# Kernel optimization log

Measured on AMD Instinct MI355X. Metric: run time of the kernel, lower is better.

Reference implementation:

```python
import jax, jax.numpy as jnp
import numpy as np

EPS = 1e-8

def squash(s, axis=-1):
    sq = jnp.sum(s * s, axis=axis, keepdims=True)
    return sq / (1.0 + sq) * s / (jnp.sqrt(sq) + EPS)

def setup_inputs() -> dict:
    key = jax.random.key(0)
    k1, k2 = jax.random.split(key)
    B, in_caps, in_dim = 256, 1152, 8
    num_caps, dim_caps = 10, 16
    x = jax.random.normal(k1, (B, in_caps, in_dim), dtype=jnp.float32)
    W = 0.01 * jax.random.normal(k2, (num_caps, in_caps, dim_caps, in_dim), dtype=jnp.float32)
    return {"x": x, "W": W}

def reference(x, W, num_routing=3):
    # u_hat: [B, num_caps, in_caps, dim_caps]
    u_hat = jnp.einsum('ncdi,bci->bncd', W, x)
    u_hat_det = jax.lax.stop_gradient(u_hat)
    B, N, C, D = u_hat.shape
    b = jnp.zeros((B, N, C, 1), dtype=u_hat.dtype)
    for _ in range(num_routing - 1):
        c = jax.nn.softmax(b, axis=1)                 # over num_caps
        s = jnp.sum(c * u_hat_det, axis=2)            # [B, N, D]
        v = squash(s)
        uv = jnp.einsum('bncd,bnd->bnc', u_hat_det, v)[..., None]
        b = b + uv
    c = jax.nn.softmax(b, axis=1)
    s = jnp.sum(c * u_hat, axis=2)
    v = squash(s)                                     # [B, N, D]
    return v
```

## Files before the change

kernel.cpp:

```cpp
#include <hip/hip_runtime.h>
#include <math.h>
#include <stdint.h>

#define B_N 256
#define C_N 1152
#define I_N 8
#define N_N 10
#define D_N 16

constexpr int C_PER    = 18;
constexpr int C_CHUNKS = C_N / C_PER;
constexpr int STAGE_C  = 3;
constexpr int N_STAGES = 6;
constexpr int BLOCK    = 256;

typedef short v8s __attribute__((ext_vector_type(8)));
typedef float v4f __attribute__((ext_vector_type(4)));

constexpr int POOL_BYTES = 32432;

constexpr size_t VSTG_FL = 16 * 16 * 164;
constexpr size_t PS_FL   = (size_t)C_CHUNKS * B_N * 160;
constexpr size_t WB_SH   = (size_t)C_N * 1280;
constexpr int    BAR_W   = 16 * 64;

#define GLD16(g, l)                                                         \
    __builtin_amdgcn_global_load_lds(                                       \
        (const uint32_t __attribute__((address_space(1)))*)(g),             \
        (uint32_t __attribute__((address_space(3)))*)(l), 16, 0, 0)

__device__ __forceinline__ void st16_sc1(float* p, v4f v) {
    asm volatile("global_store_dwordx4 %0, %1, off sc1"
                 :: "v"(p), "v"(v) : "memory");
}
__device__ __forceinline__ v4f ld16_sc1(const float* p) {
    v4f v;
    asm volatile("global_load_dwordx4 %0, %1, off sc1\n\t"
                 "s_waitcnt vmcnt(0)"
                 : "=&v"(v) : "v"(p) : "memory");
    return v;
}

__device__ __forceinline__ uint32_t cvtpk(float a, float b) {
    uint32_t r;
    asm("v_cvt_pk_bf16_f32 %0, %1, %2" : "=v"(r) : "v"(a), "v"(b));
    return r;
}
__device__ __forceinline__ float bf2f(short s) {
    return __uint_as_float(((uint32_t)(uint16_t)s) << 16);
}

__global__ __launch_bounds__(BLOCK)
void conv_all(const float* __restrict__ W, short* __restrict__ Wb,
              uint32_t* __restrict__ bar)
{
    if (blockIdx.x == 0) {
        for (int i = threadIdx.x; i < BAR_W; i += BLOCK) bar[i] = 0u;
    }
    const int c0 = blockIdx.x * 8;
    const int cc = threadIdx.x >> 5;
    const int k4 = threadIdx.x & 31;
    const float4* W4 = (const float4*)W;
    uint2* dst = (uint2*)Wb;
    for (int n = 0; n < N_N; ++n) {
        float4 v = W4[(size_t)n * 36864 + (size_t)(c0 + cc) * 32 + k4];
        dst[(((size_t)(c0 + cc) * 1280 + n * 128) >> 2) + k4] =
            make_uint2(cvtpk(v.x, v.y), cvtpk(v.z, v.w));
    }
}

__device__ __forceinline__ void gbar(uint32_t* bar, int group, uint32_t expect)
{
    asm volatile("s_waitcnt vmcnt(0) lgkmcnt(0)" ::: "memory");
    __syncthreads();
    if (threadIdx.x == 0) {
        uint32_t* cnt = &bar[group * 64];
        uint32_t* ph  = &bar[group * 64 + 32];
        uint32_t a = __hip_atomic_fetch_add(cnt, 1u, __ATOMIC_RELAXED,
                                            __HIP_MEMORY_SCOPE_AGENT);
        if (a == 63u) {
            __hip_atomic_store(cnt, 0u, __ATOMIC_RELAXED,
                               __HIP_MEMORY_SCOPE_AGENT);
            asm volatile("s_waitcnt vmcnt(0)" ::: "memory");
            __hip_atomic_fetch_add(ph, 1u, __ATOMIC_RELAXED,
                                   __HIP_MEMORY_SCOPE_AGENT);
        }
        while (__hip_atomic_load(ph, __ATOMIC_RELAXED,
                                 __HIP_MEMORY_SCOPE_AGENT) < expect)
            __builtin_amdgcn_s_sleep(2);
    }
    __syncthreads();
}

template <bool FIRST>
__device__ __forceinline__ void route_core(
    short* wbuf, const short* xs, float* vst, float* cfl, float* comb,
    const short* __restrict__ Wb, const float* __restrict__ vstG,
    float* __restrict__ p_s, int chunk, int btile)
{
    const int tid  = threadIdx.x;
    const int wv   = tid >> 6;
    const int lane = tid & 63;
    const int b    = lane & 15;
    const int quad = lane >> 4;
    const int gb0  = btile * 16;
    const int c0   = chunk * C_PER;

    if (!FIRST) {
        const float* src = vstG + (size_t)btile * 2624;
        const int f0 = tid;
        const int f1 = tid + 256;
        int f2 = tid + 512; f2 = (f2 < 656) ? f2 : 655;
        v4f t0, t1, t2;
        asm volatile(
            "global_load_dwordx4 %0, %3, off sc1\n\t"
            "global_load_dwordx4 %1, %4, off sc1\n\t"
            "global_load_dwordx4 %2, %5, off sc1\n\t"
            "s_waitcnt vmcnt(0)"
            : "=&v"(t0), "=&v"(t1), "=&v"(t2)
            : "v"(src + f0 * 4), "v"(src + f1 * 4), "v"(src + f2 * 4)
            : "memory");
        *(v4f*)((char*)vst + f0 * 16) = t0;
        *(v4f*)((char*)vst + f1 * 16) = t1;
        *(v4f*)((char*)vst + f2 * 16) = t2;
    }
    #pragma unroll
    for (int s0 = 0; s0 < 2; ++s0) {
        const char* src = (const char*)(Wb + (size_t)(c0 + s0 * STAGE_C) * 1280);
        char* dst = (char*)(wbuf + s0 * (STAGE_C * 1280));
        #pragma unroll
        for (int it = 0; it < 2; ++it) {
            int f = tid + BLOCK * it;
            if (f < 480) GLD16(src + f * 16, dst + f * 16);
        }
        asm volatile("" ::: "memory");
    }
    asm volatile("s_waitcnt vmcnt(2) lgkmcnt(0)" ::: "memory");
    __builtin_amdgcn_s_barrier();

    const int ncnt = (wv < 2) ? 3 : 2;
    v4f sacc[3];
    sacc[0] = (v4f){0.f, 0.f, 0.f, 0.f};
    sacc[1] = (v4f){0.f, 0.f, 0.f, 0.f};
    sacc[2] = (v4f){0.f, 0.f, 0.f, 0.f};

    for (int st = 0; st < N_STAGES; ++st) {
        const short* Ws = wbuf + (st & 1) * (STAGE_C * 1280);

        if (st >= 1 && st < N_STAGES - 1) {
            const char* src =
                (const char*)(Wb + (size_t)(c0 + (st + 1) * STAGE_C) * 1280);
            char* dst = (char*)(wbuf + ((st + 1) & 1) * (STAGE_C * 1280));
            #pragma unroll
            for (int it = 0; it < 2; ++it) {
                int f = tid + BLOCK * it;
                if (f < 480) GLD16(src + f * 16, dst + f * 16);
            }
            asm volatile("" ::: "memory");
        }

        if (!FIRST) {
            #pragma unroll
            for (int k = 0; k < 8; ++k) {
                const int idx = wv + 4 * k;
                if (idx < 30) {
                    const int c = idx / 10;
                    const int n = idx - c * 10;
                    v8s wa = {0, 0, 0, 0, 0, 0, 0, 0};
                    if (quad == 0)
                        wa = *(const v8s*)(Ws + c * 1280 + n * 128 + b * 8);
                    const v8s xb =
                        *(const v8s*)(xs + (st * STAGE_C + c) * 128 + b * 8);
                    v4f u = __builtin_amdgcn_mfma_f32_16x16x32_bf16(
                        wa, xb, (v4f){0.f, 0.f, 0.f, 0.f}, 0, 0, 0);
                    const float4 v4 =
                        *(const float4*)(vst + b * 164 + n * 16 + quad * 4);
                    float l = u[0] * v4.x + u[1] * v4.y + u[2] * v4.z + u[3] * v4.w;
                    l += __shfl_xor(l, 16);
                    l += __shfl_xor(l, 32);
                    const float e1 = __expf(l);
                    if (quad == 0) cfl[c * 163 + n * 16 + b] = e1;
                }
            }
            asm volatile("s_waitcnt lgkmcnt(0)" ::: "memory");
            __builtin_amdgcn_s_barrier();
        }

        {
            const bool valid = (quad < STAGE_C);
            const int  cl    = valid ? quad : 0;
            const v8s xq =
                *(const v8s*)(xs + (st * STAGE_C + cl) * 128 + b * 8);
            float xf[8];
            #pragma unroll
            for (int j = 0; j < 8; ++j) xf[j] = bf2f(xq[j]);

            if (FIRST) {
                union { v8s s; uint32_t u[4]; } zu;
                zu.u[0] = cvtpk(0.1f * xf[0], 0.1f * xf[1]);
                zu.u[1] = cvtpk(0.1f * xf[2], 0.1f * xf[3]);
                zu.u[2] = cvtpk(0.1f * xf[4], 0.1f * xf[5]);
                zu.u[3] = cvtpk(0.1f * xf[6], 0.1f * xf[7]);
                #pragma unroll
                for (int jj = 0; jj < 3; ++jj) {
                    if (jj < ncnt) {
                        const int n = wv + 4 * jj;
                        v8s wa = {0, 0, 0, 0, 0, 0, 0, 0};
                        if (valid)
                            wa = *(const v8s*)(Ws + cl * 1280 + n * 128 + b * 8);
                        sacc[jj] = __builtin_amdgcn_mfma_f32_16x16x32_bf16(
                            wa, zu.s, sacc[jj], 0, 0, 0);
                    }
                }
            } else {
                float Z = 0.f;
                #pragma unroll
                for (int n = 0; n < N_N; ++n) Z += cfl[cl * 163 + n * 16 + b];
                const float rzv = __builtin_amdgcn_rcpf(Z);
                #pragma unroll
                for (int jj = 0; jj < 3; ++jj) {
                    if (jj < ncnt) {
                        const int n = wv + 4 * jj;
                        const float cv = cfl[cl * 163 + n * 16 + b] * rzv;
                        union { v8s s; uint32_t u[4]; } zu;
                        zu.u[0] = cvtpk(cv * xf[0], cv * xf[1]);
                        zu.u[1] = cvtpk(cv * xf[2], cv * xf[3]);
                        zu.u[2] = cvtpk(cv * xf[4], cv * xf[5]);
                        zu.u[3] = cvtpk(cv * xf[6], cv * xf[7]);
                        v8s wa = {0, 0, 0, 0, 0, 0, 0, 0};
                        if (valid)
                            wa = *(const v8s*)(Ws + cl * 1280 + n * 128 + b * 8);
                        sacc[jj] = __builtin_amdgcn_mfma_f32_16x16x32_bf16(
                            wa, zu.s, sacc[jj], 0, 0, 0);
                    }
                }
            }
        }

        asm volatile("s_waitcnt vmcnt(0) lgkmcnt(0)" ::: "memory");
        __builtin_amdgcn_s_barrier();
    }

    #pragma unroll
    for (int jj = 0; jj < 3; ++jj) {
        if (jj < ncnt) {
            const int n = wv + 4 * jj;
            #pragma unroll
            for (int r = 0; r < 4; ++r)
                comb[b * 164 + n * 16 + quad * 4 + r] = sacc[jj][r];
        }
    }
    __syncthreads();
    #pragma unroll
    for (int it = 0; it < 3; ++it) {
        int f = tid + BLOCK * it;
        if (f < 640) {
            int e = f * 4;
            int bb = e / 160, rem = e - bb * 160;
            v4f v = *(const v4f*)(comb + bb * 164 + rem);
            st16_sc1(&p_s[((size_t)chunk * B_N + gb0 + bb) * 160 + rem], v);
        }
    }
}

__device__ __forceinline__ void reduce_core(const float* __restrict__ p_s,
                                            float* __restrict__ vstG,
                                            float* __restrict__ out,
                                            int phase, int chunk, int btile)
{
    const int wv   = threadIdx.x >> 6;
    const int lane = threadIdx.x & 63;
    const int k    = wv * 64 + chunk;
    if (k >= 160) return;
    const int bb = k / 10, n = k - bb * 10;
    const int g  = (btile * 16 + bb) * 10 + n;
    const int q = lane & 3;
    const int h = lane >> 2;

    const float* base = p_s + (size_t)g * D_N + q * 4;
    v4f a0, a1, a2, a3;
    asm volatile(
        "global_load_dwordx4 %0, %4, off sc1\n\t"
        "global_load_dwordx4 %1, %5, off sc1\n\t"
        "global_load_dwordx4 %2, %6, off sc1\n\t"
        "global_load_dwordx4 %3, %7, off sc1\n\t"
        "s_waitcnt vmcnt(0)"
        : "=&v"(a0), "=&v"(a1), "=&v"(a2), "=&v"(a3)
        : "v"(base + (size_t)(h)      * 40960),
          "v"(base + (size_t)(h + 16) * 40960),
          "v"(base + (size_t)(h + 32) * 40960),
          "v"(base + (size_t)(h + 48) * 40960)
        : "memory");
    v4f s = a0 + a1 + a2 + a3;

    #pragma unroll
    for (int off = 4; off < 64; off <<= 1) {
        s[0] += __shfl_xor(s[0], off);
        s[1] += __shfl_xor(s[1], off);
        s[2] += __shfl_xor(s[2], off);
        s[3] += __shfl_xor(s[3], off);
    }
    float sq = s[0] * s[0] + s[1] * s[1] + s[2] * s[2] + s[3] * s[3];
    sq += __shfl_xor(sq, 1);
    sq += __shfl_xor(sq, 2);

    const float scale = (sq / (1.f + sq)) / (sqrtf(sq) + 1e-8f);
    const v4f v = {scale * s[0], scale * s[1], scale * s[2], scale * s[3]};

    if (h == 0) {
        if (phase == 2) {
            *(float4*)(&out[(size_t)g * D_N + q * 4]) =
                make_float4(v[0], v[1], v[2], v[3]);
        } else {
            float* vp = vstG + (size_t)btile * 2624 + bb * 164 + n * 16 + q * 4;
            if (phase == 0) {
                st16_sc1(vp, v);
            } else {
                v4f o = ld16_sc1(vp);
                st16_sc1(vp, o + v);
            }
        }
    }
}

__global__ __launch_bounds__(BLOCK, 4)
void fused_route(const float* __restrict__ x, const short* __restrict__ Wb,
                 float* __restrict__ vstG, float* __restrict__ p_s,
                 float* __restrict__ out, uint32_t* bar)
{
    __shared__ __align__(16) char pool[POOL_BYTES];
    short* wbuf = (short*)pool;
    short* xs   = (short*)(pool + 15360);
    float* vst  = (float*)(pool + 19968);
    float* cfl  = (float*)(pool + 30464);
    float* comb = (float*)pool;

    const int chunk = blockIdx.x;
    const int btile = blockIdx.y;
    const int tid   = threadIdx.x;
    const int gb0   = btile * 16;
    const int c0    = chunk * C_PER;

    {
        const float4* x4 = (const float4*)x;
        #pragma unroll
        for (int it = 0; it < 3; ++it) {
            int f = tid + BLOCK * it;
            if (f < 576) {
                int b = f / 36, r = f - b * 36;
                float4 v = x4[(size_t)(gb0 + b) * 2304 + c0 * 2 + r];
                int cp = r >> 1, i0 = (r & 1) * 4;
                *(uint2*)(xs + cp * 128 + b * 8 + i0) =
                    make_uint2(cvtpk(v.x, v.y), cvtpk(v.z, v.w));
            }
        }
        asm volatile("s_waitcnt vmcnt(0)" ::: "memory");
    }

    route_core<true>(wbuf, xs, vst, cfl, comb, Wb, vstG, p_s, chunk, btile);
    gbar(bar, btile, 1);
    reduce_core(p_s, vstG, out, 0, chunk, btile);
    gbar(bar, btile, 2);

    #pragma unroll 1
    for (int pass = 1; pass <= 2; ++pass) {
        route_core<false>(wbuf, xs, vst, cfl, comb, Wb, vstG, p_s, chunk, btile);
        gbar(bar, btile, (uint32_t)(2 * pass + 1));
        reduce_core(p_s, vstG, out, pass == 2 ? 2 : 1, chunk, btile);
        if (pass == 1) gbar(bar, btile, 4);
    }
}

extern "C" void kernel_launch(void* const* d_in, const int* in_sizes, int n_in,
                              void* d_out, int out_size, void* d_ws, size_t ws_size,
                              hipStream_t stream)
{
    const float* x = (const float*)d_in[0];
    const float* W = (const float*)d_in[1];
    float* out  = (float*)d_out;

    float* vstG = (float*)d_ws;
    float* p_s  = vstG + VSTG_FL;
    short* Wb   = (short*)(p_s + PS_FL);
    uint32_t* bar = (uint32_t*)(Wb + WB_SH);

    conv_all<<<dim3(144), BLOCK, 0, stream>>>(W, Wb, bar);
    fused_route<<<dim3(C_CHUNKS, 16), BLOCK, 0, stream>>>(x, Wb, vstG, p_s, out, bar);
}
```

Measured before the change: 122.5 us.

## Replace partial-sum buffer and reduce phase with global float atomics

Each block now atomically adds its per-chunk partial sums into a shared per-routing-pass accumulator instead of writing them to a large partial buffer that a separate reduce phase later sums. This removes the reduce phase and halves the number of grid barriers per pass. Each block recomputes squash redundantly into LDS from the accumulated sums, and only 40 chunks wait at the final barrier to write the output. In exchange there is heavy atomic contention: 64 chunks add into the same 2560 floats per batch tile, and float atomics make the summation order nondeterministic.

```diff
diff --git a/kernel.cpp b/kernel.cpp
--- a/kernel.cpp
+++ b/kernel.cpp
@@ -19,26 +19,18 @@
 
 constexpr int POOL_BYTES = 32432;
 
-constexpr size_t VSTG_FL = 16 * 16 * 164;
-constexpr size_t PS_FL   = (size_t)C_CHUNKS * B_N * 160;
-constexpr size_t WB_SH   = (size_t)C_N * 1280;
-constexpr int    BAR_W   = 16 * 64;
+constexpr int    SG_FL = 16 * 16 * 164;
+constexpr size_t WB_SH = (size_t)C_N * 1280;
+constexpr int    BAR_W = 16 * 64;
 
 #define GLD16(g, l)                                                         \
     __builtin_amdgcn_global_load_lds(                                       \
         (const uint32_t __attribute__((address_space(1)))*)(g),             \
         (uint32_t __attribute__((address_space(3)))*)(l), 16, 0, 0)
 
-__device__ __forceinline__ void st16_sc1(float* p, v4f v) {
-    asm volatile("global_store_dwordx4 %0, %1, off sc1"
+__device__ __forceinline__ void atom_add_sc1(float* p, float v) {
+    asm volatile("global_atomic_add_f32 %0, %1, off sc1"
                  :: "v"(p), "v"(v) : "memory");
-}
-__device__ __forceinline__ v4f ld16_sc1(const float* p) {
-    v4f v;
-    asm volatile("global_load_dwordx4 %0, %1, off sc1\n\t"
-                 "s_waitcnt vmcnt(0)"
-                 : "=&v"(v) : "v"(p) : "memory");
-    return v;
 }
 
 __device__ __forceinline__ uint32_t cvtpk(float a, float b) {
@@ -52,11 +44,12 @@
 
 __global__ __launch_bounds__(BLOCK)
 void conv_all(const float* __restrict__ W, short* __restrict__ Wb,
-              uint32_t* __restrict__ bar)
-{
-    if (blockIdx.x == 0) {
-        for (int i = threadIdx.x; i < BAR_W; i += BLOCK) bar[i] = 0u;
-    }
+              float* __restrict__ sG, uint32_t* __restrict__ bar)
+{
+    const int gid = blockIdx.x * BLOCK + threadIdx.x;
+    if (gid < BAR_W) bar[gid] = 0u;
+    for (int i = gid; i < 3 * SG_FL; i += 144 * BLOCK) sG[i] = 0.f;
+
     const int c0 = blockIdx.x * 8;
     const int cc = threadIdx.x >> 5;
     const int k4 = threadIdx.x & 31;
@@ -69,7 +62,8 @@
     }
 }
 
-__device__ __forceinline__ void gbar(uint32_t* bar, int group, uint32_t expect)
+__device__ __forceinline__ void gbar(uint32_t* bar, int group, uint32_t expect,
+                                     bool wait)
 {
     asm volatile("s_waitcnt vmcnt(0) lgkmcnt(0)" ::: "memory");
     __syncthreads();
@@ -85,45 +79,66 @@
             __hip_atomic_fetch_add(ph, 1u, __ATOMIC_RELAXED,
                                    __HIP_MEMORY_SCOPE_AGENT);
         }
-        while (__hip_atomic_load(ph, __ATOMIC_RELAXED,
-                                 __HIP_MEMORY_SCOPE_AGENT) < expect)
-            __builtin_amdgcn_s_sleep(2);
+        if (wait) {
+            while (__hip_atomic_load(ph, __ATOMIC_RELAXED,
+                                     __HIP_MEMORY_SCOPE_AGENT) < expect)
+                __builtin_amdgcn_s_sleep(2);
+        }
+    }
+    __syncthreads();
+}
+
+template <bool ACC>
+__device__ __forceinline__ void squash_into_vst(const float* __restrict__ sGrp,
+                                                float* vst, int tid)
+{
+    if (tid < 160) {
+        const int bb = tid / 10, n = tid - bb * 10;
+        const float* rp = sGrp + bb * 164 + n * 16;
+        v4f r0, r1, r2, r3;
+        asm volatile(
+            "global_load_dwordx4 %0, %4, off sc1\n\t"
+            "global_load_dwordx4 %1, %5, off sc1\n\t"
+            "global_load_dwordx4 %2, %6, off sc1\n\t"
+            "global_load_dwordx4 %3, %7, off sc1\n\t"
+            "s_waitcnt vmcnt(0)"
+            : "=&v"(r0), "=&v"(r1), "=&v"(r2), "=&v"(r3)
+            : "v"(rp), "v"(rp + 4), "v"(rp + 8), "v"(rp + 12)
+            : "memory");
+        float sq = r0[0]*r0[0] + r0[1]*r0[1] + r0[2]*r0[2] + r0[3]*r0[3]
+                 + r1[0]*r1[0] + r1[1]*r1[1] + r1[2]*r1[2] + r1[3]*r1[3]
+                 + r2[0]*r2[0] + r2[1]*r2[1] + r2[2]*r2[2] + r2[3]*r2[3]
+                 + r3[0]*r3[0] + r3[1]*r3[1] + r3[2]*r3[2] + r3[3]*r3[3];
+        const float scale = (sq / (1.f + sq)) / (sqrtf(sq) + 1e-8f);
+        float* vp = vst + bb * 164 + n * 16;
+        if (ACC) {
+            *(v4f*)(vp)      += r0 * scale;
+            *(v4f*)(vp + 4)  += r1 * scale;
+            *(v4f*)(vp + 8)  += r2 * scale;
+            *(v4f*)(vp + 12) += r3 * scale;
+        } else {
+            *(v4f*)(vp)      = r0 * scale;
+            *(v4f*)(vp + 4)  = r1 * scale;
+            *(v4f*)(vp + 8)  = r2 * scale;
+            *(v4f*)(vp + 12) = r3 * scale;
+        }
     }
     __syncthreads();
 }
 
 template <bool FIRST>
 __device__ __forceinline__ void route_core(
-    short* wbuf, const short* xs, float* vst, float* cfl, float* comb,
-    const short* __restrict__ Wb, const float* __restrict__ vstG,
-    float* __restrict__ p_s, int chunk, int btile)
+    short* wbuf, const short* xs, const float* vst, float* cfl,
+    const short* __restrict__ Wb, float* __restrict__ sGout,
+    int chunk, int btile)
 {
     const int tid  = threadIdx.x;
     const int wv   = tid >> 6;
     const int lane = tid & 63;
     const int b    = lane & 15;
     const int quad = lane >> 4;
-    const int gb0  = btile * 16;
     const int c0   = chunk * C_PER;
 
-    if (!FIRST) {
-        const float* src = vstG + (size_t)btile * 2624;
-        const int f0 = tid;
-        const int f1 = tid + 256;
-        int f2 = tid + 512; f2 = (f2 < 656) ? f2 : 655;
-        v4f t0, t1, t2;
-        asm volatile(
-            "global_load_dwordx4 %0, %3, off sc1\n\t"
-            "global_load_dwordx4 %1, %4, off sc1\n\t"
-            "global_load_dwordx4 %2, %5, off sc1\n\t"
-            "s_waitcnt vmcnt(0)"
-            : "=&v"(t0), "=&v"(t1), "=&v"(t2)
-            : "v"(src + f0 * 4), "v"(src + f1 * 4), "v"(src + f2 * 4)
-            : "memory");
-        *(v4f*)((char*)vst + f0 * 16) = t0;
-        *(v4f*)((char*)vst + f1 * 16) = t1;
-        *(v4f*)((char*)vst + f2 * 16) = t2;
-    }
     #pragma unroll
     for (int s0 = 0; s0 < 2; ++s0) {
         const char* src = (const char*)(Wb + (size_t)(c0 + s0 * STAGE_C) * 1280);
@@ -241,105 +256,39 @@
         __builtin_amdgcn_s_barrier();
     }
 
+    float* sgb = sGout + (size_t)btile * 2624;
     #pragma unroll
     for (int jj = 0; jj < 3; ++jj) {
         if (jj < ncnt) {
             const int n = wv + 4 * jj;
+            float* p = sgb + b * 164 + n * 16 + quad * 4;
             #pragma unroll
             for (int r = 0; r < 4; ++r)
-                comb[b * 164 + n * 16 + quad * 4 + r] = sacc[jj][r];
-        }
-    }
-    __syncthreads();
-    #pragma unroll
-    for (int it = 0; it < 3; ++it) {
-        int f = tid + BLOCK * it;
-        if (f < 640) {
-            int e = f * 4;
-            int bb = e / 160, rem = e - bb * 160;
-            v4f v = *(const v4f*)(comb + bb * 164 + rem);
-            st16_sc1(&p_s[((size_t)chunk * B_N + gb0 + bb) * 160 + rem], v);
-        }
-    }
-}
-
-__device__ __forceinline__ void reduce_core(const float* __restrict__ p_s,
-                                            float* __restrict__ vstG,
-                                            float* __restrict__ out,
-                                            int phase, int chunk, int btile)
-{
-    const int wv   = threadIdx.x >> 6;
-    const int lane = threadIdx.x & 63;
-    const int k    = wv * 64 + chunk;
-    if (k >= 160) return;
-    const int bb = k / 10, n = k - bb * 10;
-    const int g  = (btile * 16 + bb) * 10 + n;
-    const int q = lane & 3;
-    const int h = lane >> 2;
-
-    const float* base = p_s + (size_t)g * D_N + q * 4;
-    v4f a0, a1, a2, a3;
-    asm volatile(
-        "global_load_dwordx4 %0, %4, off sc1\n\t"
-        "global_load_dwordx4 %1, %5, off sc1\n\t"
-        "global_load_dwordx4 %2, %6, off sc1\n\t"
-        "global_load_dwordx4 %3, %7, off sc1\n\t"
-        "s_waitcnt vmcnt(0)"
-        : "=&v"(a0), "=&v"(a1), "=&v"(a2), "=&v"(a3)
-        : "v"(base + (size_t)(h)      * 40960),
-          "v"(base + (size_t)(h + 16) * 40960),
-          "v"(base + (size_t)(h + 32) * 40960),
-          "v"(base + (size_t)(h + 48) * 40960)
-        : "memory");
-    v4f s = a0 + a1 + a2 + a3;
-
-    #pragma unroll
-    for (int off = 4; off < 64; off <<= 1) {
-        s[0] += __shfl_xor(s[0], off);
-        s[1] += __shfl_xor(s[1], off);
-        s[2] += __shfl_xor(s[2], off);
-        s[3] += __shfl_xor(s[3], off);
-    }
-    float sq = s[0] * s[0] + s[1] * s[1] + s[2] * s[2] + s[3] * s[3];
-    sq += __shfl_xor(sq, 1);
-    sq += __shfl_xor(sq, 2);
-
-    const float scale = (sq / (1.f + sq)) / (sqrtf(sq) + 1e-8f);
-    const v4f v = {scale * s[0], scale * s[1], scale * s[2], scale * s[3]};
-
-    if (h == 0) {
-        if (phase == 2) {
-            *(float4*)(&out[(size_t)g * D_N + q * 4]) =
-                make_float4(v[0], v[1], v[2], v[3]);
-        } else {
-            float* vp = vstG + (size_t)btile * 2624 + bb * 164 + n * 16 + q * 4;
-            if (phase == 0) {
-                st16_sc1(vp, v);
-            } else {
-                v4f o = ld16_sc1(vp);
-                st16_sc1(vp, o + v);
-            }
+                atom_add_sc1(p + r, sacc[jj][r]);
         }
     }
 }
 
 __global__ __launch_bounds__(BLOCK, 4)
 void fused_route(const float* __restrict__ x, const short* __restrict__ Wb,
-                 float* __restrict__ vstG, float* __restrict__ p_s,
-                 float* __restrict__ out, uint32_t* bar)
+                 float* __restrict__ sG, float* __restrict__ out,
+                 uint32_t* bar)
 {
     __shared__ __align__(16) char pool[POOL_BYTES];
     short* wbuf = (short*)pool;
     short* xs   = (short*)(pool + 15360);
     float* vst  = (float*)(pool + 19968);
     float* cfl  = (float*)(pool + 30464);
-    float* comb = (float*)pool;
 
     const int chunk = blockIdx.x;
     const int btile = blockIdx.y;
     const int tid   = threadIdx.x;
     const int gb0   = btile * 16;
     const int c0    = chunk * C_PER;
+
+    float* sG0 = sG;
+    float* sG1 = sG + SG_FL;
+    float* sG2 = sG + 2 * SG_FL;
 
     {
         const float4* x4 = (const float4*)x;
@@ -357,17 +306,33 @@
         asm volatile("s_waitcnt vmcnt(0)" ::: "memory");
     }
 
-    route_core<true>(wbuf, xs, vst, cfl, comb, Wb, vstG, p_s, chunk, btile);
-    gbar(bar, btile, 1);
-    reduce_core(p_s, vstG, out, 0, chunk, btile);
-    gbar(bar, btile, 2);
-
-    #pragma unroll 1
-    for (int pass = 1; pass <= 2; ++pass) {
-        route_core<false>(wbuf, xs, vst, cfl, comb, Wb, vstG, p_s, chunk, btile);
-        gbar(bar, btile, (uint32_t)(2 * pass + 1));
-        reduce_core(p_s, vstG, out, pass == 2 ? 2 : 1, chunk, btile);
-        if (pass == 1) gbar(bar, btile, 4);
+    route_core<true>(wbuf, xs, vst, cfl, Wb, sG0, chunk, btile);
+    gbar(bar, btile, 1, true);
+
+    squash_into_vst<false>(sG0 + (size_t)btile * 2624, vst, tid);
+    route_core<false>(wbuf, xs, vst, cfl, Wb, sG1, chunk, btile);
+    gbar(bar, btile, 2, true);
+
+    squash_into_vst<true>(sG1 + (size_t)btile * 2624, vst, tid);
+    route_core<false>(wbuf, xs, vst, cfl, Wb, sG2, chunk, btile);
+
+    const bool writer = (chunk < 40);
+    gbar(bar, btile, 3, writer);
+    if (writer && tid < 64) {
+        const int k  = chunk * 4 + (tid >> 4);
+        const int bb = k / 10, n = k - bb * 10, d = tid & 15;
+        const float* sp = sG2 + (size_t)btile * 2624 + bb * 164 + n * 16 + d;
+        float sv;
+        asm volatile("global_load_dword %0, %1, off sc1\n\t"
+                     "s_waitcnt vmcnt(0)"
+                     : "=&v"(sv) : "v"(sp) : "memory");
+        float sq = sv * sv;
+        sq += __shfl_xor(sq, 1);
+        sq += __shfl_xor(sq, 2);
+        sq += __shfl_xor(sq, 4);
+        sq += __shfl_xor(sq, 8);
+        const float scale = (sq / (1.f + sq)) / (sqrtf(sq) + 1e-8f);
+        out[((size_t)(gb0 + bb) * 10 + n) * 16 + d] = scale * sv;
     }
 }
 
@@ -379,11 +344,10 @@
     const float* W = (const float*)d_in[1];
     float* out  = (float*)d_out;
 
-    float* vstG = (float*)d_ws;
-    float* p_s  = vstG + VSTG_FL;
-    short* Wb   = (short*)(p_s + PS_FL);
+    float* sG = (float*)d_ws;
+    short* Wb = (short*)(sG + 3 * SG_FL);
     uint32_t* bar = (uint32_t*)(Wb + WB_SH);
 
-    conv_all<<<dim3(144), BLOCK, 0, stream>>>(W, Wb, bar);
-    fused_route<<<dim3(C_CHUNKS, 16), BLOCK, 0, stream>>>(x, Wb, vstG, p_s, out, bar);
-}
+    conv_all<<<dim3(144), BLOCK, 0, stream>>>(W, Wb, sG, bar);
+    fused_route<<<dim3(C_CHUNKS, 16), BLOCK, 0, stream>>>(x, Wb, sG, out, bar);
+}
```

Result: slower. 340.6 us (+178.1%).

## Prefetch next pass's W stages across grid barriers and store partial sums directly

Applied to the files above, without the earlier changes.

At the end of each routing pass, the first two W stages for the next pass are prefetched into shared memory, so the loads overlap the grid barrier and reduce phase instead of starting cold. The partial sums are also written straight from MFMA accumulators to global memory, which drops the shared-memory staging buffer and a __syncthreads. The pass loop is unrolled into explicit template instantiations to select the prestage and prefetch behaviour. The direct stores are less coalesced, and the prefetched data must stay intact in the W buffer across the reduce phase.

```diff
diff --git a/kernel.cpp b/kernel.cpp
--- a/kernel.cpp
+++ b/kernel.cpp
@@ -92,9 +92,9 @@
     __syncthreads();
 }
 
-template <bool FIRST>
+template <bool FIRST, bool PRESTAGE, bool PREFETCH>
 __device__ __forceinline__ void route_core(
-    short* wbuf, const short* xs, float* vst, float* cfl, float* comb,
+    short* wbuf, const short* xs, const float* vst_c, float* vst, float* cfl,
     const short* __restrict__ Wb, const float* __restrict__ vstG,
     float* __restrict__ p_s, int chunk, int btile)
 {
@@ -106,6 +106,22 @@
     const int gb0  = btile * 16;
     const int c0   = chunk * C_PER;
 
+    if (!PRESTAGE) {
+        #pragma unroll
+        for (int s0 = 0; s0 < 2; ++s0) {
+            const char* src =
+                (const char*)(Wb + (size_t)(c0 + s0 * STAGE_C) * 1280);
+            char* dst = (char*)(wbuf + s0 * (STAGE_C * 1280));
+            #pragma unroll
+            for (int it = 0; it < 2; ++it) {
+                int f = tid + BLOCK * it;
+                if (f < 480) GLD16(src + f * 16, dst + f * 16);
+            }
+            asm volatile("" ::: "memory");
+        }
+        asm volatile("s_waitcnt vmcnt(2) lgkmcnt(0)" ::: "memory");
+        __builtin_amdgcn_s_barrier();
+    }
     if (!FIRST) {
         const float* src = vstG + (size_t)btile * 2624;
         const int f0 = tid;
@@ -123,20 +139,9 @@
         *(v4f*)((char*)vst + f0 * 16) = t0;
         *(v4f*)((char*)vst + f1 * 16) = t1;
         *(v4f*)((char*)vst + f2 * 16) = t2;
-    }
-    #pragma unroll
-    for (int s0 = 0; s0 < 2; ++s0) {
-        const char* src = (const char*)(Wb + (size_t)(c0 + s0 * STAGE_C) * 1280);
-        char* dst = (char*)(wbuf + s0 * (STAGE_C * 1280));
-        #pragma unroll
-        for (int it = 0; it < 2; ++it) {
-            int f = tid + BLOCK * it;
-            if (f < 480) GLD16(src + f * 16, dst + f * 16);
-        }
-        asm volatile("" ::: "memory");
-    }
-    asm volatile("s_waitcnt vmcnt(2) lgkmcnt(0)" ::: "memory");
-    __builtin_amdgcn_s_barrier();
+        asm volatile("s_waitcnt lgkmcnt(0)" ::: "memory");
+        __builtin_amdgcn_s_barrier();
+    }
 
     const int ncnt = (wv < 2) ? 3 : 2;
     v4f sacc[3];
@@ -174,7 +179,7 @@
                     v4f u = __builtin_amdgcn_mfma_f32_16x16x32_bf16(
                         wa, xb, (v4f){0.f, 0.f, 0.f, 0.f}, 0, 0, 0);
                     const float4 v4 =
-                        *(const float4*)(vst + b * 164 + n * 16 + quad * 4);
+                        *(const float4*)(vst_c + b * 164 + n * 16 + quad * 4);
                     float l = u[0] * v4.x + u[1] * v4.y + u[2] * v4.z + u[3] * v4.w;
                     l += __shfl_xor(l, 16);
                     l += __shfl_xor(l, 32);
@@ -241,24 +246,27 @@
         __builtin_amdgcn_s_barrier();
     }
 
+    if (PREFETCH) {
+        #pragma unroll
+        for (int s0 = 0; s0 < 2; ++s0) {
+            const char* src =
+                (const char*)(Wb + (size_t)(c0 + s0 * STAGE_C) * 1280);
+            char* dst = (char*)(wbuf + s0 * (STAGE_C * 1280));
+            #pragma unroll
+            for (int it = 0; it < 2; ++it) {
+                int f = tid + BLOCK * it;
+                if (f < 480) GLD16(src + f * 16, dst + f * 16);
+            }
+            asm volatile("" ::: "memory");
+        }
+    }
+
     #pragma unroll
     for (int jj = 0; jj < 3; ++jj) {
         if (jj < ncnt) {
             const int n = wv + 4 * jj;
-            #pragma unroll
-            for (int r = 0; r < 4; ++r)
-                comb[b * 164 + n * 16 + quad * 4 + r] = sacc[jj][r];
-        }
-    }
-    __syncthreads();
-    #pragma unroll
-    for (int it = 0; it < 3; ++it) {
-        int f = tid + BLOCK * it;
-        if (f < 640) {
-            int e = f * 4;
-            int bb = e / 160, rem = e - bb * 160;
-            v4f v = *(const v4f*)(comb + bb * 164 + rem);
-            st16_sc1(&p_s[((size_t)chunk * B_N + gb0 + bb) * 160 + rem], v);
+            st16_sc1(&p_s[((size_t)chunk * B_N + gb0 + b) * 160 + n * 16 + quad * 4],
+                     sacc[jj]);
         }
     }
 }
@@ -333,7 +341,6 @@
     short* xs   = (short*)(pool + 15360);
     float* vst  = (float*)(pool + 19968);
     float* cfl  = (float*)(pool + 30464);
-    float* comb = (float*)pool;
 
     const int chunk = blockIdx.x;
     const int btile = blockIdx.y;
@@ -357,18 +364,22 @@
         asm volatile("s_waitcnt vmcnt(0)" ::: "memory");
     }
 
-    route_core<true>(wbuf, xs, vst, cfl, comb, Wb, vstG, p_s, chunk, btile);
+    route_core<true, false, true>(wbuf, xs, vst, vst, cfl, Wb, vstG, p_s,
+                                  chunk, btile);
     gbar(bar, btile, 1);
     reduce_core(p_s, vstG, out, 0, chunk, btile);
     gbar(bar, btile, 2);
 
-    #pragma unroll 1
-    for (int pass = 1; pass <= 2; ++pass) {
-        route_core<false>(wbuf, xs, vst, cfl, comb, Wb, vstG, p_s, chunk, btile);
-        gbar(bar, btile, (uint32_t)(2 * pass + 1));
-        reduce_core(p_s, vstG, out, pass == 2 ? 2 : 1, chunk, btile);
-        if (pass == 1) gbar(bar, btile, 4);
-    }
+    route_core<false, true, true>(wbuf, xs, vst, vst, cfl, Wb, vstG, p_s,
+                                  chunk, btile);
+    gbar(bar, btile, 3);
+    reduce_core(p_s, vstG, out, 1, chunk, btile);
+    gbar(bar, btile, 4);
+
+    route_core<false, true, false>(wbuf, xs, vst, vst, cfl, Wb, vstG, p_s,
+                                   chunk, btile);
+    gbar(bar, btile, 5);
+    reduce_core(p_s, vstG, out, 2, chunk, btile);
 }
 
 extern "C" void kernel_launch(void* const* d_in, const int* in_sizes, int n_in,
```

Result: no change. 121.6 us (-0.7%).
